# Kernel tuning notes

Hardware: AMD Instinct MI355X
Metric: run time of the kernel (lower is better)

The kernel has to match this reference:

```python
import jax, jax.numpy as jnp
import numpy as np

N = 2048      # num graph nodes (activities + places)
D = 256       # embedding_size
C = 3 * D     # cat_embedding_size
V = 2         # num variants
L = 16        # activities per variant
E = 16 * N    # edges for the encoder GNN
DEG_P = 0.0156  # adjacency density (~32 out-degree)


def setup_inputs() -> dict:
    key = jax.random.key(0)
    ks = jax.random.split(key, 6)
    embeddings = jax.random.normal(ks[0], (N, D), dtype=jnp.float32)
    W_self = jax.random.normal(ks[1], (D, D), dtype=jnp.float32) * 0.05
    W_nbr = jax.random.normal(ks[2], (D, D), dtype=jnp.float32) * 0.05
    b = jnp.zeros((D,), dtype=jnp.float32)
    variants = jax.random.randint(ks[3], (V, L), 0, N, dtype=jnp.int32)
    original = (jax.random.uniform(ks[4], (N, N)) < DEG_P).astype(jnp.int32)
    edge_index = jax.random.randint(ks[5], (2, E), 0, N, dtype=jnp.int32)
    return {"embeddings": embeddings, "W_self": W_self, "W_nbr": W_nbr, "b": b,
            "variants": variants, "original": original, "edge_index": edge_index}


def _forward(embeddings, W_self, W_nbr, b, variants, original, edge_index):
    n, d = embeddings.shape
    c = 3 * d
    dt = embeddings.dtype
    adj = original.astype(dt)              # [N,N]; adj[i,j]=1 iff edge i->j (forward star = row)
    src_e, dst_e = edge_index[0], edge_index[1]

    def encoder(x):
        # SecondEncoder approximated as one GCN-style message-passing layer
        msg = jax.ops.segment_sum(x[src_e], dst_e, num_segments=n)
        return jax.nn.relu(x @ W_self + msg @ W_nbr + b)

    def run_variant(acts):  # acts: [L] int32
        onehot = jax.nn.one_hot(acts, n, dtype=dt)                # [L,N]
        incl = jnp.flip(jnp.cumsum(jnp.flip(onehot, 0), 0), 0)    # sum_{j>=i} onehot[j]
        present_later = ((incl - onehot) > 0).astype(dt)          # set of nodes in acts[i+1:]

        def step(carry, inp):
            emb, pi, summary = carry
            a, plater = inp
            followers = adj[a]                                    # forward star of activity a
            has = jnp.any(followers > 0)
            adj_m = adj * plater[None, :]                         # edges into later-in-variant activities
            dest_cnt = adj_m.sum(axis=1)                          # |destination set| per candidate place
            dst_all = adj_m @ emb                                 # summed destination embeddings, [N,D]
            mask = jnp.where(has, ((followers > 0) & (dest_cnt > 0)).astype(dt), 0.0)
            # cat = (place_f, src_f, dst_f) per considered place
            cat = jnp.concatenate(
                [emb, jnp.broadcast_to(emb[a][None, :], emb.shape), dst_all], axis=1) * mask[:, None]
            pi = pi + cat                                         # places_info[place] += cat
            # prev_embedding_summary += places_info[place] for each considered place
            summary = summary + (mask[:, None] * pi).sum(axis=0)
            # places_info[considered] += prev_embedding_summary
            pi = pi + mask[:, None] * summary[None, :]
            emb = jnp.where(has, encoder(emb), emb)               # encoder skipped when no followers
            return (emb, pi, summary), None

        init = (embeddings, jnp.zeros((n, c), dt), jnp.zeros((c,), dt))
        (_, pi, _), _ = jax.lax.scan(step, init, (acts, present_later))
        return pi

    # variant shuffle in the original is irrelevant: embeddings reset each variant
    # and final_places_info is a sum over variants.
    return jax.vmap(run_variant)(variants).sum(axis=0)


def reference(embeddings, W_self, W_nbr, b, variants, original, edge_index):
    return _forward(embeddings, W_self, W_nbr, b, variants, original, edge_index)
```

## Files before the change

kernel.cpp:

```cpp
#include <hip/hip_runtime.h>

#define N 2048
#define D 256
#define C 768
#define V 2
#define L 16
#define NSTATE 15
#define NAPP 14
#define TCAP 256
#define FCAP 64

typedef __attribute__((ext_vector_type(8))) short bf16x8;
typedef __attribute__((ext_vector_type(4))) float f32x4;

__device__ __forceinline__ ushort bf16_rn(float x) {
  unsigned u = __float_as_uint(x);
  u += 0x7FFFu + ((u >> 16) & 1u);
  return (ushort)(u >> 16);
}
__device__ __forceinline__ float bf16_f(ushort h) {
  return __uint_as_float(((unsigned)h) << 16);
}

__device__ __forceinline__ size_t a_addr(int row, int k) {
  return ((size_t)(row >> 5) * 4 + (k >> 6)) * 2048 + (row & 31) * 64 + (k & 63);
}
__device__ __forceinline__ size_t wt_addr(int n, int k) {
  return ((size_t)(n >> 5) * 4 + (k >> 6)) * 2048 + (n & 31) * 64 + (k & 63);
}

__global__ __launch_bounds__(256) void k_init(
    const float* __restrict__ emb, const float* __restrict__ Ws,
    const float* __restrict__ Wn, float* __restrict__ states0,
    ushort* __restrict__ WtHi, ushort* __restrict__ WtLo,
    ushort* __restrict__ A0hi, ushort* __restrict__ A0lo,
    float* __restrict__ out, int* __restrict__ fillpos) {
  size_t i = (size_t)blockIdx.x * 256 + threadIdx.x;
  size_t stride = (size_t)gridDim.x * 256;
  for (size_t x = i; x < (size_t)N * D; x += stride) {
    float v = emb[x];
    states0[x] = v;
    ushort h = bf16_rn(v);
    ushort l = bf16_rn(v - bf16_f(h));
    size_t a = a_addr((int)(x >> 8), (int)(x & 255));
    A0hi[a] = h;
    A0lo[a] = l;
  }
  for (size_t x = i; x < (size_t)512 * 256; x += stride) {
    int n = (int)(x >> 8), k = (int)(x & 255);
    float v = (n < 256) ? Ws[(size_t)k * 256 + n] : Wn[(size_t)k * 256 + (n - 256)];
    ushort h = bf16_rn(v);
    size_t a = wt_addr(n, k);
    WtHi[a] = h;
    WtLo[a] = bf16_rn(v - bf16_f(h));
  }
  for (size_t x = i; x < (size_t)N * C; x += stride) out[x] = 0.f;
  for (size_t x = i; x < N; x += stride) fillpos[x] = 0;
}

__global__ __launch_bounds__(256) void k_degA(
    const int* __restrict__ ei, int E, int* __restrict__ fillpos,
    const int* __restrict__ adj, const int* __restrict__ variants,
    int* __restrict__ stepP, int* __restrict__ stepDm,
    int* __restrict__ stepCnt, int* __restrict__ hasG, int* __restrict__ tlG) {
  __shared__ int tl_sh[16];
  __shared__ int foll[FCAP], fbits[FCAP];
  __shared__ int sh_tc, sh_fcnt, sh_ecnt;
  int t = threadIdx.x;
  if (blockIdx.x < 128) {
    for (int e = blockIdx.x * 256 + t; e < E; e += 128 * 256)
      atomicAdd(&fillpos[ei[E + e]], 1);
    return;
  }
  int vi = blockIdx.x - 128;
  int v = vi / L, i = vi % L;
  int a = variants[vi];
  if (t == 0) {
    int cnt = 0;
    for (int j = i + 1; j < L; j++) {
      int x = variants[v * L + j];
      bool dup = false;
      for (int q = 0; q < cnt; q++) if (tl_sh[q] == x) dup = true;
      if (!dup) tl_sh[cnt++] = x;
    }
    sh_tc = cnt;
    sh_fcnt = 0;
    sh_ecnt = 0;
    for (int q = 0; q < cnt; q++) tlG[vi * 16 + q] = tl_sh[q];
  }
  __syncthreads();
  for (int p = t; p < N; p += 256) {
    if (adj[(size_t)a * N + p] != 0) {
      int f = atomicAdd(&sh_fcnt, 1);
      if (f < FCAP) foll[f] = p;
    }
  }
  __syncthreads();
  int fc = sh_fcnt < FCAP ? sh_fcnt : FCAP;
  int tc = sh_tc;
  for (int x = t; x < fc; x += 256) fbits[x] = 0;
  __syncthreads();
  for (int x = t; x < fc * tc; x += 256) {
    int fi = x / tc, q = x - fi * tc;
    if (adj[(size_t)foll[fi] * N + tl_sh[q]] != 0) atomicOr(&fbits[fi], 1 << q);
  }
  __syncthreads();
  for (int fi = t; fi < fc; fi += 256) {
    int bits = fbits[fi];
    if (bits) {
      int e = atomicAdd(&sh_ecnt, 1);
      stepP[vi * FCAP + e] = foll[fi];
      stepDm[vi * FCAP + e] = bits;
    }
  }
  __syncthreads();
  if (t == 0) {
    stepCnt[vi] = sh_ecnt;
    hasG[vi] = (sh_fcnt > 0);
  }
}

__global__ __launch_bounds__(256) void k_scan(int* __restrict__ fillpos,
                                              int* __restrict__ row_ptr) {
  __shared__ int part[256];
  __shared__ int base[257];
  int t = threadIdx.x;
  int v[8];
  int s = 0;
  for (int j = 0; j < 8; j++) { v[j] = fillpos[t * 8 + j]; s += v[j]; }
  part[t] = s;
  __syncthreads();
  if (t == 0) {
    int acc = 0;
    for (int q = 0; q < 256; q++) { base[q] = acc; acc += part[q]; }
    base[256] = acc;
  }
  __syncthreads();
  int acc = base[t];
  for (int j = 0; j < 8; j++) {
    row_ptr[t * 8 + j] = acc;
    fillpos[t * 8 + j] = acc;
    acc += v[j];
  }
  if (t == 255) row_ptr[N] = base[256];
}

__global__ __launch_bounds__(256) void k_fillB(
    const int* __restrict__ ei, int E, int* __restrict__ fillpos,
    int* __restrict__ csr_src,
    const int* __restrict__ stepP, const int* __restrict__ stepDm,
    const int* __restrict__ stepCnt, const int* __restrict__ hasG,
    int* __restrict__ entP, int* __restrict__ entPrev, int* __restrict__ entDm,
    int* __restrict__ offsG, int* __restrict__ kidxG, int* __restrict__ cmatG,
    int* __restrict__ lastPG, int* __restrict__ lastIG, int* __restrict__ lastMG,
    int* __restrict__ cntG) {
  __shared__ int pmask[N];
  __shared__ int sP[16][FCAP];
  __shared__ int sDm[16][FCAP];
  __shared__ int cnt[16], offs[17];
  __shared__ int cmat_sh[256];
  __shared__ int sh_u;
  int t = threadIdx.x;
  if (blockIdx.x < 128) {
    for (int e = blockIdx.x * 256 + t; e < E; e += 128 * 256) {
      int dst = ei[E + e];
      int pos = atomicAdd(&fillpos[dst], 1);
      csr_src[pos] = ei[e];
    }
    return;
  }
  int v = blockIdx.x - 128;
  for (int p = t; p < N; p += 256) pmask[p] = 0;
  for (int x = t; x < 256; x += 256) cmat_sh[x] = 0;
  if (t < 16) cnt[t] = stepCnt[v * L + t];
  if (t == 0) sh_u = 0;
  __syncthreads();
  if (t == 0) {
    int acc = 0;
    for (int i = 0; i < 16; i++) {
      offs[i] = acc < TCAP ? acc : TCAP;
      acc += cnt[i];
    }
    offs[16] = acc < TCAP ? acc : TCAP;
    cntG[v * 2 + 0] = offs[16];
    int k = 0;
    for (int i = 0; i < L; i++) {
      kidxG[v * 16 + i] = k;
      if (hasG[v * L + i]) k++;
    }
  }
  for (int x = t; x < 16 * FCAP; x += 256) {
    int i = x >> 6, f = x & 63;
    if (f < stepCnt[v * L + i]) {
      int p = stepP[(v * L + i) * FCAP + f];
      sP[i][f] = p;
      sDm[i][f] = stepDm[(v * L + i) * FCAP + f];
      atomicOr(&pmask[p], 1 << i);
    }
  }
  __syncthreads();
  for (int x = t; x < 16 * FCAP; x += 256) {
    int i = x >> 6, f = x & 63;
    if (f < cnt[i]) {
      int e = offs[i] + f;
      if (e < TCAP) {
        int p = sP[i][f];
        entP[v * TCAP + e] = p;
        entDm[v * TCAP + e] = sDm[i][f];
        int m = pmask[p] & ((1 << i) - 1);
        int prev = -1;
        if (m) {
          int j = 31 - __clz(m);
          int cj = cnt[j];
          for (int f2 = 0; f2 < cj; f2++)
            if (sP[j][f2] == p) { prev = offs[j] + f2; break; }
        }
        entPrev[v * TCAP + e] = prev;
      }
    }
  }
  __syncthreads();
  for (int p = t; p < N; p += 256) {
    int m = pmask[p];
    if (m) {
      int u = atomicAdd(&sh_u, 1);
      int j = 31 - __clz(m);
      int li = -1;
      int cj = cnt[j];
      for (int f2 = 0; f2 < cj; f2++)
        if (sP[j][f2] == p) { li = offs[j] + f2; break; }
      lastPG[v * TCAP + u] = p;
      lastIG[v * TCAP + u] = li;
      lastMG[v * TCAP + u] = m;
      int mm = m;
      while (mm) {
        int bi = __ffs(mm) - 1; mm &= mm - 1;
        int m2 = m & ((1 << bi) - 1);
        while (m2) {
          int bj = __ffs(m2) - 1; m2 &= m2 - 1;
          atomicAdd(&cmat_sh[bi * 16 + bj], 1);
        }
      }
    }
  }
  __syncthreads();
  if (t == 0) cntG[v * 2 + 1] = sh_u;
  for (int x = t; x < 256; x += 256) cmatG[v * 256 + x] = cmat_sh[x];
  for (int x = t; x < 17; x += 256) offsG[v * 17 + x] = offs[x];
}

__global__ __launch_bounds__(256) void k_gemm(
    const ushort* __restrict__ Ah, const ushort* __restrict__ Al,
    const ushort* __restrict__ Wh_g, const ushort* __restrict__ Wl_g,
    float* __restrict__ Z) {
  __shared__ __align__(16) ushort Ash[2][32][72], Asl[2][32][72];
  __shared__ __align__(16) ushort Wsh[2][32][72], Wsl[2][32][72];
  const int tid = threadIdx.x, wave = tid >> 6, lane = tid & 63;
  const int quad = lane >> 4, l16 = lane & 15;
  const int wr = wave >> 1, wc = wave & 1;
  const int mb = blockIdx.x, nb = blockIdx.y;
  const int sr = tid >> 3, sc = (tid & 7) * 8;

  f32x4 acc = {0.f, 0.f, 0.f, 0.f};
  size_t abase = (size_t)mb * 4 * 2048 + (size_t)tid * 8;
  size_t wbase = (size_t)nb * 4 * 2048 + (size_t)tid * 8;
  {
    uint4 ra  = *(const uint4*)&Ah[abase];
    uint4 rl  = *(const uint4*)&Al[abase];
    uint4 rwh = *(const uint4*)&Wh_g[wbase];
    uint4 rwl = *(const uint4*)&Wl_g[wbase];
    *(uint4*)&Ash[0][sr][sc] = ra;
    *(uint4*)&Asl[0][sr][sc] = rl;
    *(uint4*)&Wsh[0][sr][sc] = rwh;
    *(uint4*)&Wsl[0][sr][sc] = rwl;
  }
  __syncthreads();
#pragma unroll
  for (int c = 0; c < 4; c++) {
    const int rb = c & 1;
    uint4 ra, rl, rwh, rwl;
    if (c < 3) {
      size_t o = (size_t)(c + 1) * 2048;
      ra  = *(const uint4*)&Ah[abase + o];
      rl  = *(const uint4*)&Al[abase + o];
      rwh = *(const uint4*)&Wh_g[wbase + o];
      rwl = *(const uint4*)&Wl_g[wbase + o];
    }
#pragma unroll
    for (int kf = 0; kf < 2; kf++) {
      int ko = kf * 32 + quad * 8;
      bf16x8 a_h = *(const bf16x8*)&Ash[rb][wr * 16 + l16][ko];
      bf16x8 a_l = *(const bf16x8*)&Asl[rb][wr * 16 + l16][ko];
      bf16x8 w_h = *(const bf16x8*)&Wsh[rb][wc * 16 + l16][ko];
      bf16x8 w_l = *(const bf16x8*)&Wsl[rb][wc * 16 + l16][ko];
      acc = __builtin_amdgcn_mfma_f32_16x16x32_bf16(a_h, w_h, acc, 0, 0, 0);
      acc = __builtin_amdgcn_mfma_f32_16x16x32_bf16(a_h, w_l, acc, 0, 0, 0);
      acc = __builtin_amdgcn_mfma_f32_16x16x32_bf16(a_l, w_h, acc, 0, 0, 0);
    }
    if (c < 3) {
      const int wb = rb ^ 1;
      *(uint4*)&Ash[wb][sr][sc] = ra;
      *(uint4*)&Asl[wb][sr][sc] = rl;
      *(uint4*)&Wsh[wb][sr][sc] = rwh;
      *(uint4*)&Wsl[wb][sr][sc] = rwl;
      __syncthreads();
    }
  }
  int col = nb * 32 + wc * 16 + l16;
  int row0 = mb * 32 + wr * 16 + quad * 4;
#pragma unroll
  for (int r = 0; r < 4; r++)
    Z[(size_t)(row0 + r) * 512 + col] = acc[r];
}

__global__ __launch_bounds__(256) void k_comb(
    const float* __restrict__ Z, const float* __restrict__ bias,
    const int* __restrict__ row_ptr, const int* __restrict__ csr_src,
    float* __restrict__ stnext, ushort* __restrict__ NAh,
    ushort* __restrict__ NAl) {
  int row = blockIdx.x * 4 + (threadIdx.x >> 6);
  int lane = threadIdx.x & 63;
  const float4* Zp = (const float4*)Z;
  float4 acc = Zp[(size_t)row * 128 + lane];
  float4 acc2 = {0.f, 0.f, 0.f, 0.f};
  int e0 = row_ptr[row], e1 = row_ptr[row + 1];
  int e = e0;
  for (; e + 1 < e1; e += 2) {
    int s0 = csr_src[e], s1 = csr_src[e + 1];
    float4 x0 = Zp[(size_t)s0 * 128 + 64 + lane];
    float4 x1 = Zp[(size_t)s1 * 128 + 64 + lane];
    acc.x += x0.x; acc.y += x0.y; acc.z += x0.z; acc.w += x0.w;
    acc2.x += x1.x; acc2.y += x1.y; acc2.z += x1.z; acc2.w += x1.w;
  }
  if (e < e1) {
    float4 x0 = Zp[(size_t)csr_src[e] * 128 + 64 + lane];
    acc.x += x0.x; acc.y += x0.y; acc.z += x0.z; acc.w += x0.w;
  }
  float4 bv = ((const float4*)bias)[lane];
  float v0 = fmaxf(acc.x + acc2.x + bv.x, 0.f);
  float v1 = fmaxf(acc.y + acc2.y + bv.y, 0.f);
  float v2 = fmaxf(acc.z + acc2.z + bv.z, 0.f);
  float v3 = fmaxf(acc.w + acc2.w + bv.w, 0.f);
  *(float4*)(stnext + (size_t)row * D + lane * 4) = make_float4(v0, v1, v2, v3);
  ushort h0 = bf16_rn(v0), h1 = bf16_rn(v1), h2 = bf16_rn(v2), h3 = bf16_rn(v3);
  size_t ca = a_addr(row, lane * 4);
  *(ushort4*)&NAh[ca] = make_ushort4(h0, h1, h2, h3);
  *(ushort4*)&NAl[ca] = make_ushort4(
      bf16_rn(v0 - bf16_f(h0)), bf16_rn(v1 - bf16_f(h1)),
      bf16_rn(v2 - bf16_f(h2)), bf16_rn(v3 - bf16_f(h3)));
}

#define PI_LDS_BYTES (TCAP * 64 * 4 + 16 * 64 * 4 + 3 * TCAP * 4 + 17 * 4 + 16 * 4 + 256 * 4)
__global__ __launch_bounds__(64) void k_pi(
    const float* __restrict__ states, float* __restrict__ out,
    const int* __restrict__ variants,
    const int* __restrict__ entP, const int* __restrict__ entPrev,
    const int* __restrict__ entDm, const int* __restrict__ offsG,
    const int* __restrict__ kidxG, const int* __restrict__ tlG,
    const int* __restrict__ cmatG, const int* __restrict__ lastPG,
    const int* __restrict__ lastIG, const int* __restrict__ lastMG,
    const int* __restrict__ cntG) {
  extern __shared__ __align__(16) float smf[];
  float* catb = smf;
  float* S_lds = catb + TCAP * 64;
  int* eP  = (int*)(S_lds + 16 * 64);
  int* ePr = eP + TCAP;
  int* eDm = ePr + TCAP;
  int* offs = eDm + TCAP;
  int* kidx = offs + 17;
  int* tl = kidx + 16;
  int v = blockIdx.x / 12, cgi = blockIdx.x % 12;
  int grp = cgi >> 2;
  int lane = threadIdx.x;
  int cl = (cgi & 3) * 64 + lane;
  int col = cgi * 64 + lane;

  int T = cntG[v * 2 + 0], U = cntG[v * 2 + 1];
  for (int x = lane; x < T; x += 64) {
    eP[x] = entP[v * TCAP + x];
    ePr[x] = entPrev[v * TCAP + x];
    eDm[x] = entDm[v * TCAP + x];
  }
  for (int x = lane; x < 17; x += 64) offs[x] = offsG[v * 17 + x];
  if (lane < 16) kidx[lane] = kidxG[v * 16 + lane];
  for (int x = lane; x < 256; x += 64) tl[x] = tlG[v * 256 + x];
  __syncthreads();

  for (int i = 0; i < L; i++) {
    int kk = kidx[i]; if (kk > NSTATE - 1) kk = NSTATE - 1;
    const float* embS = states + (size_t)kk * N * D;
    int o0 = offs[i], o1 = offs[i + 1];
    if (grp == 0) {
      for (int e = o0; e < o1; e++)
        catb[e * 64 + lane] = embS[(size_t)eP[e] * D + cl];
    } else if (grp == 1) {
      float embA = embS[(size_t)variants[v * L + i] * D + cl];
      for (int e = o0; e < o1; e++) catb[e * 64 + lane] = embA;
    } else {
      for (int e = o0; e < o1; e++) {
        float s = 0.f;
        int b = eDm[e];
        while (b) {
          int q = __ffs(b) - 1; b &= b - 1;
          s += embS[(size_t)tl[i * 16 + q] * D + cl];
        }
        catb[e * 64 + lane] = s;
      }
    }
  }
  for (int e = 0; e < T; e++) {
    int pr = ePr[e];
    if (pr >= 0) catb[e * 64 + lane] += catb[pr * 64 + lane];
  }
  float S[16];
  float Sp = 0.f;
#pragma unroll
  for (int i = 0; i < 16; i++) {
    float a = 0.f;
    for (int e = offs[i]; e < offs[i + 1]; e++) a += catb[e * 64 + lane];
    float s = Sp + a;
#pragma unroll
    for (int j = 0; j < 16; j++)
      if (j < i) s += (float)cmatG[v * 256 + i * 16 + j] * S[j];
    S[i] = s;
    S_lds[i * 64 + lane] = s;
    Sp = s;
  }
  for (int u = 0; u < U; u++) {
    int p = lastPG[v * TCAP + u];
    int li = lastIG[v * TCAP + u];
    int m = lastMG[v * TCAP + u];
    float acc = catb[li * 64 + lane];
    while (m) {
      int q = __ffs(m) - 1; m &= m - 1;
      acc += S_lds[q * 64 + lane];
    }
    atomicAdd(&out[(size_t)p * C + col], acc);
  }
}

extern "C" void kernel_launch(void* const* d_in, const int* in_sizes, int n_in,
                              void* d_out, int out_size, void* d_ws, size_t ws_size,
                              hipStream_t stream) {
  const float* emb      = (const float*)d_in[0];
  const float* Ws       = (const float*)d_in[1];
  const float* Wn       = (const float*)d_in[2];
  const float* bias     = (const float*)d_in[3];
  const int*   variants = (const int*)d_in[4];
  const int*   adj      = (const int*)d_in[5];
  const int*   ei       = (const int*)d_in[6];
  const int    E        = in_sizes[6] / 2;
  float* out            = (float*)d_out;

  char* base = (char*)d_ws;
  float* states = (float*)base;            base += (size_t)NSTATE * N * D * 4;
  float* Z      = (float*)base;            base += (size_t)N * 512 * 4;
  ushort* WtHi  = (ushort*)base;           base += (size_t)512 * 256 * 2;
  ushort* WtLo  = (ushort*)base;           base += (size_t)512 * 256 * 2;
  ushort* A0h   = (ushort*)base;           base += (size_t)N * D * 2;
  ushort* A0l   = (ushort*)base;           base += (size_t)N * D * 2;
  ushort* A1h   = (ushort*)base;           base += (size_t)N * D * 2;
  ushort* A1l   = (ushort*)base;           base += (size_t)N * D * 2;
  int* row_ptr  = (int*)base;              base += (N + 1) * 4;
  int* fillpos  = (int*)base;              base += N * 4;
  int* csr_src  = (int*)base;              base += (size_t)E * 4;
  int* stepP    = (int*)base;              base += V * L * FCAP * 4;
  int* stepDm   = (int*)base;              base += V * L * FCAP * 4;
  int* stepCnt  = (int*)base;              base += V * L * 4;
  int* hasG     = (int*)base;              base += V * L * 4;
  int* entP     = (int*)base;              base += V * TCAP * 4;
  int* entPrev  = (int*)base;              base += V * TCAP * 4;
  int* entDm    = (int*)base;              base += V * TCAP * 4;
  int* offsG    = (int*)base;              base += V * 17 * 4;
  int* kidxG    = (int*)base;              base += V * 16 * 4;
  int* tlG      = (int*)base;              base += V * 256 * 4;
  int* cmatG    = (int*)base;              base += V * 256 * 4;
  int* lastPG   = (int*)base;              base += V * TCAP * 4;
  int* lastIG   = (int*)base;              base += V * TCAP * 4;
  int* lastMG   = (int*)base;              base += V * TCAP * 4;
  int* cntG     = (int*)base;              base += V * 2 * 4;

  hipFuncSetAttribute((const void*)k_pi,
                      hipFuncAttributeMaxDynamicSharedMemorySize, PI_LDS_BYTES);

  k_init<<<512, 256, 0, stream>>>(emb, Ws, Wn, states, WtHi, WtLo, A0h, A0l,
                                  out, fillpos);
  k_degA<<<128 + V * L, 256, 0, stream>>>(ei, E, fillpos, adj, variants,
                                          stepP, stepDm, stepCnt, hasG, tlG);
  k_scan<<<1, 256, 0, stream>>>(fillpos, row_ptr);
  k_fillB<<<128 + V, 256, 0, stream>>>(ei, E, fillpos, csr_src, stepP, stepDm,
                                       stepCnt, hasG, entP, entPrev, entDm,
                                       offsG, kidxG, cmatG, lastPG, lastIG,
                                       lastMG, cntG);

  ushort* AH[2] = {A0h, A1h};
  ushort* AL[2] = {A0l, A1l};
  for (int s = 0; s < NAPP; s++) {
    int cur = s & 1, nxt = cur ^ 1;
    k_gemm<<<dim3(64, 16), 256, 0, stream>>>(AH[cur], AL[cur], WtHi, WtLo, Z);
    k_comb<<<N / 4, 256, 0, stream>>>(Z, bias, row_ptr, csr_src,
                                      states + (size_t)(s + 1) * N * D,
                                      AH[nxt], AL[nxt]);
  }
  k_pi<<<V * 12, 64, PI_LDS_BYTES, stream>>>(states, out, variants, entP,
                                             entPrev, entDm, offsG, kidxG, tlG,
                                             cmatG, lastPG, lastIG, lastMG, cntG);
}
```

Baseline: 380.0 us.

## Fuse neighbor aggregation with next-step GEMM into one kernel per encoder step

Adds k_fused, which gathers neighbor messages, applies bias and ReLU, writes the state, splits the activations into bf16 hi/lo in LDS and immediately runs the next step's GEMM tile. Z is ping-ponged between two buffers. This halves the number of launches in the 14-step chain and removes the global round trip of the bf16 A buffers. In exchange, each of the 4 column-block groups recomputes the aggregation for its 16 rows, so gather work is repeated 4x. The GEMM tile is also smaller, with lower reuse of W.

```diff
diff --git a/kernel.cpp b/kernel.cpp
--- a/kernel.cpp
+++ b/kernel.cpp
@@ -311,6 +311,93 @@
 #pragma unroll
   for (int r = 0; r < 4; r++)
     Z[(size_t)(row0 + r) * 512 + col] = acc[r];
+}
+
+__global__ __launch_bounds__(256) void k_fused(
+    const float* __restrict__ Zprev, float* __restrict__ Znext,
+    const ushort* __restrict__ WtHi, const ushort* __restrict__ WtLo,
+    const float* __restrict__ bias, const int* __restrict__ row_ptr,
+    const int* __restrict__ csr_src, float* __restrict__ stthis) {
+  __shared__ __align__(16) ushort Ash[16][264], Asl[16][264];
+  __shared__ __align__(16) ushort Wsh[128][72], Wsl[128][72];
+  const int tid = threadIdx.x, wave = tid >> 6, lane = tid & 63;
+  const int quad = lane >> 4, l16 = lane & 15;
+  const int mb = blockIdx.x, nb = blockIdx.y;
+  const int r0 = mb * 16;
+
+  const float4* Zp = (const float4*)Zprev;
+  float4 bv = ((const float4*)bias)[lane];
+#pragma unroll
+  for (int rr = 0; rr < 4; rr++) {
+    int row = r0 + wave * 4 + rr;
+    float4 acc = Zp[(size_t)row * 128 + lane];
+    float4 acc2 = {0.f, 0.f, 0.f, 0.f};
+    int e0 = row_ptr[row], e1 = row_ptr[row + 1];
+    int e = e0;
+    for (; e + 1 < e1; e += 2) {
+      int s0 = csr_src[e], s1 = csr_src[e + 1];
+      float4 x0 = Zp[(size_t)s0 * 128 + 64 + lane];
+      float4 x1 = Zp[(size_t)s1 * 128 + 64 + lane];
+      acc.x += x0.x; acc.y += x0.y; acc.z += x0.z; acc.w += x0.w;
+      acc2.x += x1.x; acc2.y += x1.y; acc2.z += x1.z; acc2.w += x1.w;
+    }
+    if (e < e1) {
+      float4 x0 = Zp[(size_t)csr_src[e] * 128 + 64 + lane];
+      acc.x += x0.x; acc.y += x0.y; acc.z += x0.z; acc.w += x0.w;
+    }
+    float v0 = fmaxf(acc.x + acc2.x + bv.x, 0.f);
+    float v1 = fmaxf(acc.y + acc2.y + bv.y, 0.f);
+    float v2 = fmaxf(acc.z + acc2.z + bv.z, 0.f);
+    float v3 = fmaxf(acc.w + acc2.w + bv.w, 0.f);
+    if (nb == 0)
+      *(float4*)(stthis + (size_t)row * D + lane * 4) =
+          make_float4(v0, v1, v2, v3);
+    ushort h0 = bf16_rn(v0), h1 = bf16_rn(v1), h2 = bf16_rn(v2), h3 = bf16_rn(v3);
+    int ar = wave * 4 + rr;
+    *(ushort4*)&Ash[ar][lane * 4] = make_ushort4(h0, h1, h2, h3);
+    *(ushort4*)&Asl[ar][lane * 4] = make_ushort4(
+        bf16_rn(v0 - bf16_f(h0)), bf16_rn(v1 - bf16_f(h1)),
+        bf16_rn(v2 - bf16_f(h2)), bf16_rn(v3 - bf16_f(h3)));
+  }
+
+  f32x4 acc[2] = {};
+  const int swn = tid >> 3, swk = (tid & 7) * 8;
+#pragma unroll
+  for (int kc = 0; kc < 4; kc++) {
+    __syncthreads();
+#pragma unroll
+    for (int sub = 0; sub < 4; sub++) {
+      int n = nb * 128 + sub * 32;
+      size_t gb = ((size_t)(n >> 5) * 4 + kc) * 2048 + (size_t)tid * 8;
+      *(uint4*)&Wsh[sub * 32 + swn][swk] = *(const uint4*)&WtHi[gb];
+      *(uint4*)&Wsl[sub * 32 + swn][swk] = *(const uint4*)&WtLo[gb];
+    }
+    __syncthreads();
+#pragma unroll
+    for (int kf = 0; kf < 2; kf++) {
+      int ko = kc * 64 + kf * 32 + quad * 8;
+      int wo = kf * 32 + quad * 8;
+      bf16x8 a_h = *(const bf16x8*)&Ash[l16][ko];
+      bf16x8 a_l = *(const bf16x8*)&Asl[l16][ko];
+#pragma unroll
+      for (int nt = 0; nt < 2; nt++) {
+        bf16x8 w_h = *(const bf16x8*)&Wsh[wave * 32 + nt * 16 + l16][wo];
+        bf16x8 w_l = *(const bf16x8*)&Wsl[wave * 32 + nt * 16 + l16][wo];
+        acc[nt] = __builtin_amdgcn_mfma_f32_16x16x32_bf16(a_h, w_h, acc[nt], 0, 0, 0);
+        acc[nt] = __builtin_amdgcn_mfma_f32_16x16x32_bf16(a_h, w_l, acc[nt], 0, 0, 0);
+        acc[nt] = __builtin_amdgcn_mfma_f32_16x16x32_bf16(a_l, w_h, acc[nt], 0, 0, 0);
+      }
+    }
+  }
+#pragma unroll
+  for (int nt = 0; nt < 2; nt++) {
+    int col = nb * 128 + wave * 32 + nt * 16 + l16;
+#pragma unroll
+    for (int r = 0; r < 4; r++) {
+      int row = r0 + quad * 4 + r;
+      Znext[(size_t)row * 512 + col] = acc[nt][r];
+    }
+  }
 }
 
 __global__ __launch_bounds__(256) void k_comb(
@@ -454,7 +541,8 @@
 
   char* base = (char*)d_ws;
   float* states = (float*)base;            base += (size_t)NSTATE * N * D * 4;
-  float* Z      = (float*)base;            base += (size_t)N * 512 * 4;
+  float* Z0     = (float*)base;            base += (size_t)N * 512 * 4;
+  float* Z1     = (float*)base;            base += (size_t)N * 512 * 4;
   ushort* WtHi  = (ushort*)base;           base += (size_t)512 * 256 * 2;
   ushort* WtLo  = (ushort*)base;           base += (size_t)512 * 256 * 2;
   ushort* A0h   = (ushort*)base;           base += (size_t)N * D * 2;
@@ -493,15 +581,15 @@
                                        offsG, kidxG, cmatG, lastPG, lastIG,
                                        lastMG, cntG);
 
-  ushort* AH[2] = {A0h, A1h};
-  ushort* AL[2] = {A0l, A1l};
-  for (int s = 0; s < NAPP; s++) {
-    int cur = s & 1, nxt = cur ^ 1;
-    k_gemm<<<dim3(64, 16), 256, 0, stream>>>(AH[cur], AL[cur], WtHi, WtLo, Z);
-    k_comb<<<N / 4, 256, 0, stream>>>(Z, bias, row_ptr, csr_src,
-                                      states + (size_t)(s + 1) * N * D,
-                                      AH[nxt], AL[nxt]);
-  }
+  k_gemm<<<dim3(64, 16), 256, 0, stream>>>(A0h, A0l, WtHi, WtLo, Z0);
+  float* Zb[2] = {Z0, Z1};
+  for (int s = 1; s < NAPP; s++) {
+    k_fused<<<dim3(128, 4), 256, 0, stream>>>(
+        Zb[(s - 1) & 1], Zb[s & 1], WtHi, WtLo, bias, row_ptr, csr_src,
+        states + (size_t)s * N * D);
+  }
+  k_comb<<<N / 4, 256, 0, stream>>>(Zb[(NAPP - 1) & 1], bias, row_ptr, csr_src,
+                                    states + (size_t)NAPP * N * D, A1h, A1l);
   k_pi<<<V * 12, 64, PI_LDS_BYTES, stream>>>(states, out, variants, entP,
                                              entPrev, entDm, offsG, kidxG, tlG,
                                              cmatG, lastPG, lastIG, lastMG, cntG);
```

New measurement: 457.3 us. 1.2x slower.
